# Optimization experiments

Measured on AMD Instinct MI355X. Metric: run time of the kernel, lower is better.

Reference implementation:

```python
import jax, jax.numpy as jnp
import numpy as np

BN_EPS = 1e-5


def _get_normals(radius, nsample, xyz):
    # xyz: [B, N, 3] -> normals [B, N, 3] (eigenvector of smallest eigenvalue)
    B, N, _ = xyz.shape
    sq = jnp.sum(xyz * xyz, axis=-1)                      # [B, N]
    sqrdists = sq[:, :, None] + sq[:, None, :] - 2.0 * jnp.einsum('bnc,bmc->bnm', xyz, xyz)
    ar = jnp.arange(N, dtype=jnp.int32)
    group_idx = jnp.where(sqrdists > radius * radius, N, ar[None, None, :])  # [B, N, N]
    group_idx = jnp.sort(group_idx, axis=-1)[:, :, :nsample]                 # [B, N, ns]
    group_idx = jnp.where(group_idx == N, group_idx[:, :, :1], group_idx)
    group_points = jax.vmap(lambda pts, idx: pts[idx])(xyz, group_idx)       # [B, N, ns, 3]
    centered = group_points - group_points.mean(axis=2, keepdims=True)
    cov = jnp.einsum('bnsc,bnsd->bncd', centered, centered)                  # [B, N, 3, 3]
    _, eigen_vectors = jnp.linalg.eigh(cov)
    return eigen_vectors[..., 0]


def _conv_bn(h, w, b, g, be, m, v, relu=True):
    # h: [B, N, Cin]; 1x1 Conv1d == per-point linear; BN in eval mode
    h = h @ w.T + b
    h = (h - m) / jnp.sqrt(v + BN_EPS) * g + be
    return jax.nn.relu(h) if relu else h


def setup_inputs() -> dict:
    key = jax.random.key(0)
    ks = jax.random.split(key, 32)
    B, N = 4, 4096
    inp = {
        'x': jax.random.uniform(ks[0], (B, N, 3), dtype=jnp.float32),
        'small': 0.2,
        'large': 0.3,
    }
    chans = [(1, 16), (16, 32), (32, 16), (16, 1)]
    for li, (cin, cout) in enumerate(chans, start=1):
        k = 4 * li
        inp[f'w{li}'] = jax.random.normal(ks[k], (cout, cin), dtype=jnp.float32) * (1.0 / np.sqrt(cin))
        inp[f'b{li}'] = jax.random.normal(ks[k + 1], (cout,), dtype=jnp.float32) * 0.1
        inp[f'g{li}'] = jax.random.uniform(ks[k + 2], (cout,), dtype=jnp.float32) + 0.5
        inp[f'be{li}'] = jax.random.normal(ks[k + 3], (cout,), dtype=jnp.float32) * 0.1
        inp[f'm{li}'] = jnp.zeros((cout,), dtype=jnp.float32)
        inp[f'v{li}'] = jnp.ones((cout,), dtype=jnp.float32)
    return inp


def reference(x, small, large,
              w1, b1, g1, be1, m1, v1,
              w2, b2, g2, be2, m2, v2,
              w3, b3, g3, be3, m3, v3,
              w4, b4, g4, be4, m4, v4):
    xyz = x[:, :, :3]
    small_n = _get_normals(small, 32, xyz)   # [B, N, 3]
    large_n = _get_normals(large, 64, xyz)
    curvature = jnp.linalg.norm((small_n - large_n) * 0.5, axis=2)  # [B, N]
    h = curvature[..., None]                                        # [B, N, 1]
    h = _conv_bn(h, w1, b1, g1, be1, m1, v1)
    h = _conv_bn(h, w2, b2, g2, be2, m2, v2)
    h = _conv_bn(h, w3, b3, g3, be3, m3, v3)
    h = _conv_bn(h, w4, b4, g4, be4, m4, v4, relu=False)
    return h[..., 0]                                                # [B, N]
```

## Files before the change

### kernel.cpp

```cpp
#include <hip/hip_runtime.h>
#include <math.h>

#define BLAS_FMA 1
#define SYR2_VARIANT 0

#define DEV static __device__ __forceinline__

DEV float fA(float a, float b){ return __fadd_rn(a,b); }
DEV float fSb(float a, float b){ return __fsub_rn(a,b); }
DEV float fM(float a, float b){ return __fmul_rn(a,b); }
DEV float fDv(float a, float b){ return __fdiv_rn(a,b); }
DEV float fQ(float a){ return __fsqrt_rn(a); }
DEV float fF(float a, float b, float c){ return __builtin_fmaf(a,b,c); }
DEV float fSGN(float a, float b){ return copysignf(a,b); }

DEV float slapy2f(float x, float y){
  float xa=fabsf(x), ya=fabsf(y);
  float w=fmaxf(xa,ya), z=fminf(xa,ya);
  if (z==0.0f) return w;
  float t=fDv(z,w);
  return fM(w, fQ(fA(1.0f, fM(t,t))));
}

DEV void slartgf(float f, float g, float* c, float* s, float* r){
  const float safmin=1.17549435e-38f;
  const float safmax=8.50705917e+37f;
  const float rtmin=1.08420217e-19f;
  const float rtmax=6.52169543e+18f;
  float f1=fabsf(f), g1=fabsf(g);
  if (g==0.0f){ *c=1.0f; *s=0.0f; *r=f; }
  else if (f==0.0f){ *c=0.0f; *s=fSGN(1.0f,g); *r=g1; }
  else {
    if (f1>rtmin && f1<rtmax && g1>rtmin && g1<rtmax){
      float d=fQ(fA(fM(f,f), fM(g,g)));
      *c=fDv(f1,d);
      *r=fSGN(d,f);
      *s=fDv(g,*r);
    } else {
      float u=fminf(safmax, fmaxf(safmin, fmaxf(f1,g1)));
      float fs=fDv(f,u), gs=fDv(g,u);
      float d=fQ(fA(fM(fs,fs), fM(gs,gs)));
      *c=fDv(fabsf(fs), d);
      *r=fSGN(d,f);
      *s=fDv(gs,*r);
      *r=fM(*r,u);
    }
  }
}

DEV void slaev2f(float a, float b, float c, float* rt1, float* rt2, float* cs1, float* sn1){
  float sm=fA(a,c);
  float df=fSb(a,c);
  float adf=fabsf(df);
  float tb=fA(b,b);
  float ab=fabsf(tb);
  float acmx, acmn;
  if (fabsf(a)>fabsf(c)){ acmx=a; acmn=c; } else { acmx=c; acmn=a; }
  float rt;
  if (adf>ab){ float t=fDv(ab,adf); rt=fM(adf, fQ(fA(1.0f, fM(t,t)))); }
  else if (adf<ab){ float t=fDv(adf,ab); rt=fM(ab, fQ(fA(1.0f, fM(t,t)))); }
  else { rt=fM(ab, fQ(2.0f)); }
  int sgn1;
  if (sm<0.0f){
    *rt1=fM(0.5f, fSb(sm,rt)); sgn1=-1;
    *rt2=fSb(fM(fDv(acmx,*rt1),acmn), fM(fDv(b,*rt1),b));
  } else if (sm>0.0f){
    *rt1=fM(0.5f, fA(sm,rt)); sgn1=1;
    *rt2=fSb(fM(fDv(acmx,*rt1),acmn), fM(fDv(b,*rt1),b));
  } else {
    *rt1=fM(0.5f,rt); *rt2=fM(-0.5f,rt); sgn1=1;
  }
  float cs; int sgn2;
  if (df>=0.0f){ cs=fA(df,rt); sgn2=1; } else { cs=fSb(df,rt); sgn2=-1; }
  float acs=fabsf(cs);
  if (acs>ab){
    float ct=fDv(-tb,cs);
    *sn1=fDv(1.0f, fQ(fA(1.0f, fM(ct,ct))));
    *cs1=fM(ct,*sn1);
  } else {
    if (ab==0.0f){ *cs1=1.0f; *sn1=0.0f; }
    else {
      float tn=fDv(-cs,tb);
      *cs1=fDv(1.0f, fQ(fA(1.0f, fM(tn,tn))));
      *sn1=fM(tn,*cs1);
    }
  }
  if (sgn1==sgn2){ float tn=*cs1; *cs1=-(*sn1); *sn1=tn; }
}

DEV void eig3_smallest(float a00, float a10, float a20, float a11, float a21, float a22,
                       float* vout){
  const float RMIN=3.13916472e-16f;
  const float RMAX=3.18559313e+15f;
  float anrm=fmaxf(fabsf(a00), fmaxf(fabsf(a10), fmaxf(fabsf(a20),
             fmaxf(fabsf(a11), fmaxf(fabsf(a21), fabsf(a22))))));
  if (anrm>0.0f && anrm<RMIN){
    float sig=fDv(RMIN,anrm);
    a00=fM(a00,sig); a10=fM(a10,sig); a20=fM(a20,sig);
    a11=fM(a11,sig); a21=fM(a21,sig); a22=fM(a22,sig);
  } else if (anrm>RMAX){
    float sig=fDv(RMAX,anrm);
    a00=fM(a00,sig); a10=fM(a10,sig); a20=fM(a20,sig);
    a11=fM(a11,sig); a21=fM(a21,sig); a22=fM(a22,sig);
  }
  float d[3], e[2];
  float tau1=0.0f, hv2=0.0f;
  {
    float xnorm=fabsf(a20);
    if (xnorm==0.0f){
      tau1=0.0f;
      d[0]=a00; d[1]=a11; d[2]=a22;
      e[0]=a10; e[1]=a21;
    } else {
      float alpha=a10;
      float beta=-fSGN(slapy2f(alpha,xnorm), alpha);
      tau1=fDv(fSb(beta,alpha), beta);
      float rs=fDv(1.0f, fSb(alpha,beta));
      hv2=fM(a20, rs);
      float t2a=fM(a21, hv2);
#if BLAS_FMA
      float w1=fF(tau1, t2a, fM(tau1, a11));
      float w2=fF(fM(tau1,hv2), a22, fM(tau1, a21));
      float sd=fF(hv2, w2, w1);
#else
      float w1=fA(fM(tau1,a11), fM(tau1,t2a));
      float w2=fA(fM(tau1,a21), fM(fM(tau1,hv2),a22));
      float sd=fA(w1, fM(w2,hv2));
#endif
      float al2=fM(fM(-0.5f,tau1), sd);
      float nw1=fA(w1, al2);
#if BLAS_FMA
      float nw2=fF(al2, hv2, w2);
#else
      float nw2=fA(w2, fM(al2,hv2));
#endif
      w1=nw1; w2=nw2;
      float b11, b21, b22;
#if SYR2_VARIANT==0
      b11=fA(a11, fM(-2.0f, w1));
      b21=fA(a21, fF(hv2, -w1, -w2));
      b22=fA(a22, fF(hv2, -w2, fM(w2, -hv2)));
#elif SYR2_VARIANT==1
      b11=fSb(fSb(a11, w1), w1);
      b21=fSb(fF(hv2, -w1, a21), w2);
      b22=fF(w2, -hv2, fF(hv2, -w2, a22));
#else
      b11=fA(fA(a11, -w1), -w1);
      b21=fA(fA(a21, fM(hv2,-w1)), -w2);
      b22=fA(fA(a22, fM(hv2,-w2)), fM(w2,-hv2));
#endif
      d[0]=a00; d[1]=b11; d[2]=b22;
      e[0]=beta; e[1]=b21;
    }
  }
  float z[9]={1.0f,0.0f,0.0f, 0.0f,1.0f,0.0f, 0.0f,0.0f,1.0f};
  const float EPS=5.96046448e-08f;
  const float EPS2=3.55271368e-15f;
  const float SAFMIN=1.17549435e-38f;
  const float SSFMAX=3.07445735e+18f;
  const float SSFMIN=3.05175781e-05f;
  int l1=1, jtot=0; const int nmaxit=90;
  bool skip_sort=false;
  while (l1<=3){
    if (l1>1) e[l1-2]=0.0f;
    int m=3;
    for (int mm=l1; mm<=2; ++mm){
      float tst=fabsf(e[mm-1]);
      if (tst==0.0f){ m=mm; break; }
      if (tst<=fM(fM(fQ(fabsf(d[mm-1])), fQ(fabsf(d[mm]))), EPS)){ e[mm-1]=0.0f; m=mm; break; }
    }
    int l=l1, lsv=l, lend=m, lendsv=m;
    l1=m+1;
    if (lend==l) continue;
    float anorm=fabsf(d[lend-1]);
    for (int i=l; i<=lend-1; ++i){ anorm=fmaxf(anorm,fabsf(d[i-1])); anorm=fmaxf(anorm,fabsf(e[i-1])); }
    if (anorm==0.0f) continue;
    int iscale=0;
    if (anorm>SSFMAX){
      iscale=1; float mv=fDv(SSFMAX,anorm);
      for (int i=l;i<=lend;++i) d[i-1]=fM(d[i-1],mv);
      for (int i=l;i<=lend-1;++i) e[i-1]=fM(e[i-1],mv);
    } else if (anorm<SSFMIN){
      iscale=2; float mv=fDv(SSFMIN,anorm);
      for (int i=l;i<=lend;++i) d[i-1]=fM(d[i-1],mv);
      for (int i=l;i<=lend-1;++i) e[i-1]=fM(e[i-1],mv);
    }
    if (fabsf(d[lend-1])<fabsf(d[l-1])){ lend=lsv; l=lendsv; }
    if (lend>l){
      for (;;){
        int M=lend;
        if (l!=lend){
          for (int mm=l; mm<=lend-1; ++mm){
            float ee=fabsf(e[mm-1]);
            float tst=fM(ee,ee);
            if (tst<=fA(fM(fM(EPS2,fabsf(d[mm-1])), fabsf(d[mm])), SAFMIN)){ M=mm; break; }
          }
        }
        if (M<lend) e[M-1]=0.0f;
        float p=d[l-1];
        if (M==l){
          l+=1;
          if (l<=lend) continue; else break;
        }
        if (M==l+1){
          float rt1,rt2,cc,ss;
          slaev2f(d[l-1], e[l-1], d[l], &rt1,&rt2,&cc,&ss);
          for (int i=0;i<3;++i){
            float t=z[i+3*l];
            z[i+3*l]    =fSb(fM(cc,t), fM(ss,z[i+3*(l-1)]));
            z[i+3*(l-1)]=fA (fM(ss,t), fM(cc,z[i+3*(l-1)]));
          }
          d[l-1]=rt1; d[l]=rt2; e[l-1]=0.0f; l+=2;
          if (l<=lend) continue; else break;
        }
        if (jtot==nmaxit) break;
        ++jtot;
        float g=fDv(fSb(d[l],p), fM(2.0f,e[l-1]));
        float r=slapy2f(g,1.0f);
        g=fA(fSb(d[M-1],p), fDv(e[l-1], fA(g, fSGN(r,g))));
        float s=1.0f, c=1.0f; p=0.0f;
        float cst[2], sst[2];
        for (int i=M-1; i>=l; --i){
          float f=fM(s,e[i-1]);
          float bb=fM(c,e[i-1]);
          slartgf(g,f,&c,&s,&r);
          if (i!=M-1) e[i]=r;
          g=fSb(d[i],p);
          r=fA(fM(fSb(d[i-1],g),s), fM(fM(2.0f,c),bb));
          p=fM(s,r);
          d[i]=fA(g,p);
          g=fSb(fM(c,r),bb);
          cst[i-l]=c; sst[i-l]=-s;
        }
        int nr=M-l;
        for (int j=nr; j>=1; --j){
          float ct=cst[j-1], st=sst[j-1];
          if (ct!=1.0f || st!=0.0f){
            int c0=(l-1)+(j-1);
            for (int i=0;i<3;++i){
              float t=z[i+3*(c0+1)];
              z[i+3*(c0+1)]=fSb(fM(ct,t), fM(st,z[i+3*c0]));
              z[i+3*c0]    =fA (fM(st,t), fM(ct,z[i+3*c0]));
            }
          }
        }
        d[l-1]=fSb(d[l-1],p);
        e[l-1]=g;
      }
    } else {
      for (;;){
        int M=lend;
        if (l!=lend){
          for (int mm=l; mm>=lend+1; --mm){
            float ee=fabsf(e[mm-2]);
            float tst=fM(ee,ee);
            if (tst<=fA(fM(fM(EPS2,fabsf(d[mm-1])), fabsf(d[mm-2])), SAFMIN)){ M=mm; break; }
          }
        }
        if (M>lend) e[M-2]=0.0f;
        float p=d[l-1];
        if (M==l){
          l-=1;
          if (l>=lend) continue; else break;
        }
        if (M==l-1){
          float rt1,rt2,cc,ss;
          slaev2f(d[l-2], e[l-2], d[l-1], &rt1,&rt2,&cc,&ss);
          for (int i=0;i<3;++i){
            float t=z[i+3*(l-1)];
            z[i+3*(l-1)]=fSb(fM(cc,t), fM(ss,z[i+3*(l-2)]));
            z[i+3*(l-2)]=fA (fM(ss,t), fM(cc,z[i+3*(l-2)]));
          }
          d[l-2]=rt1; d[l-1]=rt2; e[l-2]=0.0f; l-=2;
          if (l>=lend) continue; else break;
        }
        if (jtot==nmaxit) break;
        ++jtot;
        float g=fDv(fSb(d[l-2],p), fM(2.0f,e[l-2]));
        float r=slapy2f(g,1.0f);
        g=fA(fSb(d[M-1],p), fDv(e[l-2], fA(g, fSGN(r,g))));
        float s=1.0f, c=1.0f; p=0.0f;
        float cst[2], sst[2];
        for (int i=M; i<=l-1; ++i){
          float f=fM(s,e[i-1]);
          float bb=fM(c,e[i-1]);
          slartgf(g,f,&c,&s,&r);
          if (i!=M) e[i-2]=r;
          g=fSb(d[i-1],p);
          r=fA(fM(fSb(d[i],g),s), fM(fM(2.0f,c),bb));
          p=fM(s,r);
          d[i-1]=fA(g,p);
          g=fSb(fM(c,r),bb);
          cst[i-M]=c; sst[i-M]=s;
        }
        int nr=l-M;
        for (int j=1; j<=nr; ++j){
          float ct=cst[j-1], st=sst[j-1];
          if (ct!=1.0f || st!=0.0f){
            int c0=(M-1)+(j-1);
            for (int i=0;i<3;++i){
              float t=z[i+3*(c0+1)];
              z[i+3*(c0+1)]=fSb(fM(ct,t), fM(st,z[i+3*c0]));
              z[i+3*c0]    =fA(fM(st,t), fM(ct,z[i+3*c0]));
            }
          }
        }
        d[l-1]=fSb(d[l-1],p);
        e[l-2]=g;
      }
    }
    if (iscale==1){
      float mv=fDv(anorm,SSFMAX);
      for (int i=lsv;i<=lendsv;++i) d[i-1]=fM(d[i-1],mv);
      for (int i=lsv;i<=lendsv-1;++i) e[i-1]=fM(e[i-1],mv);
    } else if (iscale==2){
      float mv=fDv(anorm,SSFMIN);
      for (int i=lsv;i<=lendsv;++i) d[i-1]=fM(d[i-1],mv);
      for (int i=lsv;i<=lendsv-1;++i) e[i-1]=fM(e[i-1],mv);
    }
    if (jtot>=nmaxit){ skip_sort=true; break; }
  }
  if (!skip_sort){
    for (int ii=2; ii<=3; ++ii){
      int i=ii-1, k=i; float p=d[i-1];
      for (int j=ii; j<=3; ++j) if (d[j-1]<p){ k=j; p=d[j-1]; }
      if (k!=i){
        d[k-1]=d[i-1]; d[i-1]=p;
        for (int row=0; row<3; ++row){
          float t=z[row+3*(i-1)]; z[row+3*(i-1)]=z[row+3*(k-1)]; z[row+3*(k-1)]=t;
        }
      }
    }
  }
  float z0=z[0], z1=z[1], z2=z[2];
  if (tau1!=0.0f){
#if BLAS_FMA
    float wv=fF(hv2, z2, z1);
    float t2=fM(-tau1, wv);
    z1=fA(z1, t2);
    z2=fF(t2, hv2, z2);
#else
    float wv=fA(z1, fM(z2,hv2));
    float t2=fM(-tau1, wv);
    z1=fA(z1, t2);
    z2=fA(z2, fM(hv2,t2));
#endif
  }
  vout[0]=z0; vout[1]=z1; vout[2]=z2;
}

struct KP {
  const float* x; const float* rs; const float* rl;
  const float *w1,*b1,*g1,*be1,*m1,*v1;
  const float *w2,*b2,*g2,*be2,*m2,*v2;
  const float *w3,*b3,*g3,*be3,*m3,*v3;
  const float *w4,*b4,*g4,*be4,*m4,*v4;
  float* out;
};

#define WS_STRIDE 128

__global__ __launch_bounds__(64) void scan_kernel(const float* __restrict__ x,
                                                  const float* __restrict__ rsp,
                                                  const float* __restrict__ rlp,
                                                  unsigned short* __restrict__ ws){
  const int lane=threadIdx.x;
  const int pt=blockIdx.x;
  const int b=pt>>12, n=pt&4095;
  const float* P=x+(size_t)b*(4096*3);
  const double rds=rint((double)rsp[0]*1e7)/1e7;
  const double rdl=rint((double)rlp[0]*1e7)/1e7;
  const float rr_s=(float)(rds*rds);
  const float rr_l=(float)(rdl*rdl);
  const float px=P[3*n], py=P[3*n+1], pz=P[3*n+2];
  const float sqn=fA(fA(fM(px,px),fM(py,py)),fM(pz,pz));
  unsigned short* w=ws+(size_t)pt*WS_STRIDE;
  int cs=0, cl=0;
  for (int c=0;c<64;++c){
    int j=c*64+lane;
    float qx=P[3*j], qy=P[3*j+1], qz=P[3*j+2];
    float sqj=fA(fA(fM(qx,qx),fM(qy,qy)),fM(qz,qz));
    float dot=fA(fA(fM(px,qx),fM(py,qy)),fM(pz,qz));
    float d2=fSb(fA(sqn,sqj), fM(2.0f,dot));
    bool pl=!(d2>rr_l);
    bool ps=!(d2>rr_s);
    unsigned long long bl=__ballot(pl);
    unsigned long long bs=__ballot(ps);
    unsigned long long ltm=(1ull<<lane)-1ull;
    int posl=cl+__popcll(bl&ltm);
    int poss=cs+__popcll(bs&ltm);
    if (pl&&posl<64) w[posl]=(unsigned short)j;
    if (ps&&poss<32) w[64+poss]=(unsigned short)j;
    cl+=__popcll(bl); if(cl>64) cl=64;
    cs+=__popcll(bs); if(cs>32) cs=32;
    if (cs>=32&&cl>=64) break;
  }
  if (lane==0){ w[96]=(unsigned short)cl; w[97]=(unsigned short)cs; }
}

__global__ __launch_bounds__(64) void moments_kernel(const float* __restrict__ x,
                                                     const unsigned short* __restrict__ ws,
                                                     float* __restrict__ covB){
  __shared__ float sP[4096*3];
  __shared__ unsigned int sWu[64*65];
  const int lane=threadIdx.x;
  const int base=blockIdx.x*64;
  const int b=base>>12;
  const float* P=x+(size_t)b*(4096*3);
  {
    const float4* src=(const float4*)P;
    float4* dst=(float4*)sP;
    for (int i=lane;i<4096*3/4;i+=64) dst[i]=src[i];
  }
  {
    const unsigned int* wsrc=(const unsigned int*)(ws+(size_t)base*WS_STRIDE);
    for (int i=lane;i<64*64;i+=64){
      int row=i>>6, col=i&63;
      sWu[row*65+col]=wsrc[i];
    }
  }
  __syncthreads();

  const unsigned short* sW16=(const unsigned short*)sWu;
  const int rbase=lane*130;
  const int cln=sW16[rbase+96], csn=sW16[rbase+97];
  const int j0l=sW16[rbase+0],  j0s=sW16[rbase+64];

  float ssx=0.0f,ssy=0.0f,ssz=0.0f, slx=0.0f,sly=0.0f,slz=0.0f;
#pragma unroll 16
  for (int k=0;k<32;++k){
    int idx=(k<csn)?(int)sW16[rbase+64+k]:j0s;
    ssx=fA(ssx,sP[3*idx]); ssy=fA(ssy,sP[3*idx+1]); ssz=fA(ssz,sP[3*idx+2]);
  }
#pragma unroll 16
  for (int k=0;k<64;++k){
    int idx=(k<cln)?(int)sW16[rbase+k]:j0l;
    slx=fA(slx,sP[3*idx]); sly=fA(sly,sP[3*idx+1]); slz=fA(slz,sP[3*idx+2]);
  }
  const float msx=fDv(ssx,32.0f), msy=fDv(ssy,32.0f), msz=fDv(ssz,32.0f);
  const float mlx=fDv(slx,64.0f), mly=fDv(sly,64.0f), mlz=fDv(slz,64.0f);

  float sc0=0,sc1=0,sc2=0,sc3=0,sc4=0,sc5=0;
#pragma unroll 16
  for (int k=0;k<32;++k){
    int idx=(k<csn)?(int)sW16[rbase+64+k]:j0s;
    float cx=fSb(sP[3*idx],msx), cy=fSb(sP[3*idx+1],msy), cz=fSb(sP[3*idx+2],msz);
    sc0=fA(sc0,fM(cx,cx)); sc1=fA(sc1,fM(cy,cx)); sc2=fA(sc2,fM(cz,cx));
    sc3=fA(sc3,fM(cy,cy)); sc4=fA(sc4,fM(cz,cy)); sc5=fA(sc5,fM(cz,cz));
  }
  float lc0=0,lc1=0,lc2=0,lc3=0,lc4=0,lc5=0;
#pragma unroll 16
  for (int k=0;k<64;++k){
    int idx=(k<cln)?(int)sW16[rbase+k]:j0l;
    float cx=fSb(sP[3*idx],mlx), cy=fSb(sP[3*idx+1],mly), cz=fSb(sP[3*idx+2],mlz);
    lc0=fA(lc0,fM(cx,cx)); lc1=fA(lc1,fM(cy,cx)); lc2=fA(lc2,fM(cz,cx));
    lc3=fA(lc3,fM(cy,cy)); lc4=fA(lc4,fM(cz,cy)); lc5=fA(lc5,fM(cz,cz));
  }

  float* cb=covB+(size_t)(base+lane)*12;
  cb[0]=sc0; cb[1]=sc1; cb[2]=sc2; cb[3]=sc3; cb[4]=sc4; cb[5]=sc5;
  cb[6]=lc0; cb[7]=lc1; cb[8]=lc2; cb[9]=lc3; cb[10]=lc4; cb[11]=lc5;
}

__global__ __launch_bounds__(64) void eigmlp_kernel(KP kp, const float* __restrict__ covB){
  __shared__ float sN[32][3];
  const int lane=threadIdx.x;
  const int g=lane>>1;
  const int t=blockIdx.x*32+g;
  const int p=t>>1, which=t&1;
  const float* cb=covB+(size_t)p*12+which*6;
  float v[3];
  eig3_smallest(cb[0],cb[1],cb[2],cb[3],cb[4],cb[5],v);
  if ((lane&1)==0){ sN[g][0]=v[0]; sN[g][1]=v[1]; sN[g][2]=v[2]; }
  __syncthreads();

  if (lane<16){
    const int pt=blockIdx.x*16+lane;
    const float* sn=sN[2*lane];
    const float* ln=sN[2*lane+1];
    float dx=fM(fSb(sn[0],ln[0]),0.5f);
    float dy=fM(fSb(sn[1],ln[1]),0.5f);
    float dz=fM(fSb(sn[2],ln[2]),0.5f);
    float curv=fQ(fA(fA(fM(dx,dx),fM(dy,dy)),fM(dz,dz)));

    float h1[16];
#pragma unroll
    for (int j=0;j<16;++j){
      float a0=fA(fM(kp.w1[j],curv), kp.b1[j]);
      a0=fA(fM(fDv(fSb(a0,kp.m1[j]), fQ(fA(kp.v1[j],1e-5f))), kp.g1[j]), kp.be1[j]);
      h1[j]=fmaxf(a0,0.0f);
    }
    float h2[32];
#pragma unroll
    for (int j=0;j<32;++j){
      float a0=0.0f;
#pragma unroll
      for (int k=0;k<16;++k) a0=fF(h1[k], kp.w2[j*16+k], a0);
      a0=fA(a0, kp.b2[j]);
      a0=fA(fM(fDv(fSb(a0,kp.m2[j]), fQ(fA(kp.v2[j],1e-5f))), kp.g2[j]), kp.be2[j]);
      h2[j]=fmaxf(a0,0.0f);
    }
    float h3[16];
#pragma unroll
    for (int j=0;j<16;++j){
      float a0=0.0f;
#pragma unroll
      for (int k=0;k<32;++k) a0=fF(h2[k], kp.w3[j*32+k], a0);
      a0=fA(a0, kp.b3[j]);
      a0=fA(fM(fDv(fSb(a0,kp.m3[j]), fQ(fA(kp.v3[j],1e-5f))), kp.g3[j]), kp.be3[j]);
      h3[j]=fmaxf(a0,0.0f);
    }
    float o=0.0f;
#pragma unroll
    for (int k=0;k<16;++k) o=fF(h3[k], kp.w4[k], o);
    o=fA(o, kp.b4[0]);
    o=fA(fM(fDv(fSb(o,kp.m4[0]), fQ(fA(kp.v4[0],1e-5f))), kp.g4[0]), kp.be4[0]);
    kp.out[pt]=o;
  }
}

__global__ __launch_bounds__(256) void freq_kernel(KP kp){
  __shared__ float sP[4096*3];
  __shared__ float sSq[4096];
  __shared__ unsigned short sIdxL[64][66];
  __shared__ unsigned short sIdxS[64][34];
  __shared__ unsigned char sCntL[64], sCntS[64];
  const int tid=threadIdx.x;
  const int lane=tid&63, wid=tid>>6;
  const int b=blockIdx.x>>6;
  const int n0=(blockIdx.x&63)*64;
  const float* P=kp.x+(size_t)b*(4096*3);
  for (int i=tid;i<4096*3;i+=256) sP[i]=P[i];
  for (int j=tid;j<4096;j+=256){
    float qx=P[3*j],qy=P[3*j+1],qz=P[3*j+2];
    sSq[j]=fA(fA(fM(qx,qx),fM(qy,qy)),fM(qz,qz));
  }
  __syncthreads();
  const double rds=rint((double)kp.rs[0]*1e7)/1e7;
  const double rdl=rint((double)kp.rl[0]*1e7)/1e7;
  const float rr_s=(float)(rds*rds);
  const float rr_l=(float)(rdl*rdl);
  for (int pi=0; pi<16; ++pi){
    const int pl_i=wid*16+pi;
    const int n=n0+pl_i;
    const float px=sP[3*n], py=sP[3*n+1], pz=sP[3*n+2];
    const float sqn=sSq[n];
    int cs=0, cl=0;
    for (int c=0;c<64;++c){
      int j=c*64+lane;
      float dot=fA(fA(fM(px,sP[3*j]),fM(py,sP[3*j+1])),fM(pz,sP[3*j+2]));
      float d2=fSb(fA(sqn,sSq[j]), fM(2.0f,dot));
      bool pl_=!(d2>rr_l);
      bool ps_=!(d2>rr_s);
      unsigned long long bl=__ballot(pl_);
      unsigned long long bs=__ballot(ps_);
      unsigned long long ltm=(1ull<<lane)-1ull;
      int posl=cl+__popcll(bl&ltm);
      int poss=cs+__popcll(bs&ltm);
      if (pl_&&posl<64) sIdxL[pl_i][posl]=(unsigned short)j;
      if (ps_&&poss<32) sIdxS[pl_i][poss]=(unsigned short)j;
      cl+=__popcll(bl); if(cl>64) cl=64;
      cs+=__popcll(bs); if(cs>32) cs=32;
      if (cs>=32&&cl>=64) break;
    }
    if (lane==0){ sCntL[pl_i]=(unsigned char)cl; sCntS[pl_i]=(unsigned char)cs; }
  }
  __syncthreads();
  if (lane<16){
    const int pl_i=wid*16+lane;
    const int ptg=blockIdx.x*64+pl_i;
    const int csn=sCntS[pl_i], cln=sCntL[pl_i];
    const int j0s=sIdxS[pl_i][0], j0l=sIdxL[pl_i][0];
    float ssx=0.0f,ssy=0.0f,ssz=0.0f, slx=0.0f,sly=0.0f,slz=0.0f;
    for (int k=0;k<32;++k){
      int idx=(k<csn)?(int)sIdxS[pl_i][k]:j0s;
      ssx=fA(ssx,sP[3*idx]); ssy=fA(ssy,sP[3*idx+1]); ssz=fA(ssz,sP[3*idx+2]);
    }
    for (int k=0;k<64;++k){
      int idx=(k<cln)?(int)sIdxL[pl_i][k]:j0l;
      slx=fA(slx,sP[3*idx]); sly=fA(sly,sP[3*idx+1]); slz=fA(slz,sP[3*idx+2]);
    }
    const float msx=fDv(ssx,32.0f), msy=fDv(ssy,32.0f), msz=fDv(ssz,32.0f);
    const float mlx=fDv(slx,64.0f), mly=fDv(sly,64.0f), mlz=fDv(slz,64.0f);
    float sc0=0,sc1=0,sc2=0,sc3=0,sc4=0,sc5=0;
    for (int k=0;k<32;++k){
      int idx=(k<csn)?(int)sIdxS[pl_i][k]:j0s;
      float cx=fSb(sP[3*idx],msx), cy=fSb(sP[3*idx+1],msy), cz=fSb(sP[3*idx+2],msz);
      sc0=fA(sc0,fM(cx,cx)); sc1=fA(sc1,fM(cy,cx)); sc2=fA(sc2,fM(cz,cx));
      sc3=fA(sc3,fM(cy,cy)); sc4=fA(sc4,fM(cz,cy)); sc5=fA(sc5,fM(cz,cz));
    }
    float lc0=0,lc1=0,lc2=0,lc3=0,lc4=0,lc5=0;
    for (int k=0;k<64;++k){
      int idx=(k<cln)?(int)sIdxL[pl_i][k]:j0l;
      float cx=fSb(sP[3*idx],mlx), cy=fSb(sP[3*idx+1],mly), cz=fSb(sP[3*idx+2],mlz);
      lc0=fA(lc0,fM(cx,cx)); lc1=fA(lc1,fM(cy,cx)); lc2=fA(lc2,fM(cz,cx));
      lc3=fA(lc3,fM(cy,cy)); lc4=fA(lc4,fM(cz,cy)); lc5=fA(lc5,fM(cz,cz));
    }
    float snv[3], lnv[3];
    eig3_smallest(sc0,sc1,sc2,sc3,sc4,sc5, snv);
    eig3_smallest(lc0,lc1,lc2,lc3,lc4,lc5, lnv);
    float dx=fM(fSb(snv[0],lnv[0]),0.5f);
    float dy=fM(fSb(snv[1],lnv[1]),0.5f);
    float dz=fM(fSb(snv[2],lnv[2]),0.5f);
    float curv=fQ(fA(fA(fM(dx,dx),fM(dy,dy)),fM(dz,dz)));
    float h1[16];
#pragma unroll
    for (int j=0;j<16;++j){
      float a0=fA(fM(kp.w1[j],curv), kp.b1[j]);
      a0=fA(fM(fDv(fSb(a0,kp.m1[j]), fQ(fA(kp.v1[j],1e-5f))), kp.g1[j]), kp.be1[j]);
      h1[j]=fmaxf(a0,0.0f);
    }
    float h2[32];
#pragma unroll
    for (int j=0;j<32;++j){
      float a0=0.0f;
#pragma unroll
      for (int k=0;k<16;++k) a0=fF(h1[k], kp.w2[j*16+k], a0);
      a0=fA(a0, kp.b2[j]);
      a0=fA(fM(fDv(fSb(a0,kp.m2[j]), fQ(fA(kp.v2[j],1e-5f))), kp.g2[j]), kp.be2[j]);
      h2[j]=fmaxf(a0,0.0f);
    }
    float h3[16];
#pragma unroll
    for (int j=0;j<16;++j){
      float a0=0.0f;
#pragma unroll
      for (int k=0;k<32;++k) a0=fF(h2[k], kp.w3[j*32+k], a0);
      a0=fA(a0, kp.b3[j]);
      a0=fA(fM(fDv(fSb(a0,kp.m3[j]), fQ(fA(kp.v3[j],1e-5f))), kp.g3[j]), kp.be3[j]);
      h3[j]=fmaxf(a0,0.0f);
    }
    float o=0.0f;
#pragma unroll
    for (int k=0;k<16;++k) o=fF(h3[k], kp.w4[k], o);
    o=fA(o, kp.b4[0]);
    o=fA(fM(fDv(fSb(o,kp.m4[0]), fQ(fA(kp.v4[0],1e-5f))), kp.g4[0]), kp.be4[0]);
    kp.out[ptg]=o;
  }
}

extern "C" void kernel_launch(void* const* d_in, const int* in_sizes, int n_in,
                              void* d_out, int out_size, void* d_ws, size_t ws_size,
                              hipStream_t stream){
  (void)n_in; (void)out_size;
  KP kp;
  kp.x  =(const float*)d_in[0];
  kp.rs =(const float*)d_in[1];
  kp.rl =(const float*)d_in[2];
  kp.w1 =(const float*)d_in[3];  kp.b1 =(const float*)d_in[4];  kp.g1 =(const float*)d_in[5];
  kp.be1=(const float*)d_in[6];  kp.m1 =(const float*)d_in[7];  kp.v1 =(const float*)d_in[8];
  kp.w2 =(const float*)d_in[9];  kp.b2 =(const float*)d_in[10]; kp.g2 =(const float*)d_in[11];
  kp.be2=(const float*)d_in[12]; kp.m2 =(const float*)d_in[13]; kp.v2 =(const float*)d_in[14];
  kp.w3 =(const float*)d_in[15]; kp.b3 =(const float*)d_in[16]; kp.g3 =(const float*)d_in[17];
  kp.be3=(const float*)d_in[18]; kp.m3 =(const float*)d_in[19]; kp.v3 =(const float*)d_in[20];
  kp.w4 =(const float*)d_in[21]; kp.b4 =(const float*)d_in[22]; kp.g4 =(const float*)d_in[23];
  kp.be4=(const float*)d_in[24]; kp.m4 =(const float*)d_in[25]; kp.v4 =(const float*)d_in[26];
  kp.out=(float*)d_out;
  const int BN=in_sizes[0]/3;
  const size_t ws_need=(size_t)BN*(256+48);
  if (ws_size>=ws_need){
    unsigned short* wsA=(unsigned short*)d_ws;
    float* covB=(float*)((char*)d_ws + (size_t)BN*256);
    scan_kernel<<<BN, 64, 0, stream>>>(kp.x, kp.rs, kp.rl, wsA);
    moments_kernel<<<BN/64, 64, 0, stream>>>(kp.x, wsA, covB);
    eigmlp_kernel<<<BN/16, 64, 0, stream>>>(kp, covB);
  } else {
    freq_kernel<<<BN/64, 256, 0, stream>>>(kp);
  }
}
```

Baseline: 195.0 us.

## Drop multi-kernel workspace path and always launch fused freq kernel

Removes the scan/moments/eig-MLP three-kernel pipeline that staged neighbor indices and covariances through global workspace, and always launches the single fused kernel. This avoids workspace round trips and extra launches. In exchange it has fewer blocks (one per 64 points) and more work per block, which may underuse the GPU.

```diff
diff --git a/kernel.cpp b/kernel.cpp
--- a/kernel.cpp
+++ b/kernel.cpp
@@ -358,167 +358,6 @@
   float* out;
 };
 
-#define WS_STRIDE 128
-
-__global__ __launch_bounds__(64) void scan_kernel(const float* __restrict__ x,
-                                                  const float* __restrict__ rsp,
-                                                  const float* __restrict__ rlp,
-                                                  unsigned short* __restrict__ ws){
-  const int lane=threadIdx.x;
-  const int pt=blockIdx.x;
-  const int b=pt>>12, n=pt&4095;
-  const float* P=x+(size_t)b*(4096*3);
-  const double rds=rint((double)rsp[0]*1e7)/1e7;
-  const double rdl=rint((double)rlp[0]*1e7)/1e7;
-  const float rr_s=(float)(rds*rds);
-  const float rr_l=(float)(rdl*rdl);
-  const float px=P[3*n], py=P[3*n+1], pz=P[3*n+2];
-  const float sqn=fA(fA(fM(px,px),fM(py,py)),fM(pz,pz));
-  unsigned short* w=ws+(size_t)pt*WS_STRIDE;
-  int cs=0, cl=0;
-  for (int c=0;c<64;++c){
-    int j=c*64+lane;
-    float qx=P[3*j], qy=P[3*j+1], qz=P[3*j+2];
-    float sqj=fA(fA(fM(qx,qx),fM(qy,qy)),fM(qz,qz));
-    float dot=fA(fA(fM(px,qx),fM(py,qy)),fM(pz,qz));
-    float d2=fSb(fA(sqn,sqj), fM(2.0f,dot));
-    bool pl=!(d2>rr_l);
-    bool ps=!(d2>rr_s);
-    unsigned long long bl=__ballot(pl);
-    unsigned long long bs=__ballot(ps);
-    unsigned long long ltm=(1ull<<lane)-1ull;
-    int posl=cl+__popcll(bl&ltm);
-    int poss=cs+__popcll(bs&ltm);
-    if (pl&&posl<64) w[posl]=(unsigned short)j;
-    if (ps&&poss<32) w[64+poss]=(unsigned short)j;
-    cl+=__popcll(bl); if(cl>64) cl=64;
-    cs+=__popcll(bs); if(cs>32) cs=32;
-    if (cs>=32&&cl>=64) break;
-  }
-  if (lane==0){ w[96]=(unsigned short)cl; w[97]=(unsigned short)cs; }
-}
-
-__global__ __launch_bounds__(64) void moments_kernel(const float* __restrict__ x,
-                                                     const unsigned short* __restrict__ ws,
-                                                     float* __restrict__ covB){
-  __shared__ float sP[4096*3];
-  __shared__ unsigned int sWu[64*65];
-  const int lane=threadIdx.x;
-  const int base=blockIdx.x*64;
-  const int b=base>>12;
-  const float* P=x+(size_t)b*(4096*3);
-  {
-    const float4* src=(const float4*)P;
-    float4* dst=(float4*)sP;
-    for (int i=lane;i<4096*3/4;i+=64) dst[i]=src[i];
-  }
-  {
-    const unsigned int* wsrc=(const unsigned int*)(ws+(size_t)base*WS_STRIDE);
-    for (int i=lane;i<64*64;i+=64){
-      int row=i>>6, col=i&63;
-      sWu[row*65+col]=wsrc[i];
-    }
-  }
-  __syncthreads();
-
-  const unsigned short* sW16=(const unsigned short*)sWu;
-  const int rbase=lane*130;
-  const int cln=sW16[rbase+96], csn=sW16[rbase+97];
-  const int j0l=sW16[rbase+0],  j0s=sW16[rbase+64];
-
-  float ssx=0.0f,ssy=0.0f,ssz=0.0f, slx=0.0f,sly=0.0f,slz=0.0f;
-#pragma unroll 16
-  for (int k=0;k<32;++k){
-    int idx=(k<csn)?(int)sW16[rbase+64+k]:j0s;
-    ssx=fA(ssx,sP[3*idx]); ssy=fA(ssy,sP[3*idx+1]); ssz=fA(ssz,sP[3*idx+2]);
-  }
-#pragma unroll 16
-  for (int k=0;k<64;++k){
-    int idx=(k<cln)?(int)sW16[rbase+k]:j0l;
-    slx=fA(slx,sP[3*idx]); sly=fA(sly,sP[3*idx+1]); slz=fA(slz,sP[3*idx+2]);
-  }
-  const float msx=fDv(ssx,32.0f), msy=fDv(ssy,32.0f), msz=fDv(ssz,32.0f);
-  const float mlx=fDv(slx,64.0f), mly=fDv(sly,64.0f), mlz=fDv(slz,64.0f);
-
-  float sc0=0,sc1=0,sc2=0,sc3=0,sc4=0,sc5=0;
-#pragma unroll 16
-  for (int k=0;k<32;++k){
-    int idx=(k<csn)?(int)sW16[rbase+64+k]:j0s;
-    float cx=fSb(sP[3*idx],msx), cy=fSb(sP[3*idx+1],msy), cz=fSb(sP[3*idx+2],msz);
-    sc0=fA(sc0,fM(cx,cx)); sc1=fA(sc1,fM(cy,cx)); sc2=fA(sc2,fM(cz,cx));
-    sc3=fA(sc3,fM(cy,cy)); sc4=fA(sc4,fM(cz,cy)); sc5=fA(sc5,fM(cz,cz));
-  }
-  float lc0=0,lc1=0,lc2=0,lc3=0,lc4=0,lc5=0;
-#pragma unroll 16
-  for (int k=0;k<64;++k){
-    int idx=(k<cln)?(int)sW16[rbase+k]:j0l;
-    float cx=fSb(sP[3*idx],mlx), cy=fSb(sP[3*idx+1],mly), cz=fSb(sP[3*idx+2],mlz);
-    lc0=fA(lc0,fM(cx,cx)); lc1=fA(lc1,fM(cy,cx)); lc2=fA(lc2,fM(cz,cx));
-    lc3=fA(lc3,fM(cy,cy)); lc4=fA(lc4,fM(cz,cy)); lc5=fA(lc5,fM(cz,cz));
-  }
-
-  float* cb=covB+(size_t)(base+lane)*12;
-  cb[0]=sc0; cb[1]=sc1; cb[2]=sc2; cb[3]=sc3; cb[4]=sc4; cb[5]=sc5;
-  cb[6]=lc0; cb[7]=lc1; cb[8]=lc2; cb[9]=lc3; cb[10]=lc4; cb[11]=lc5;
-}
-
-__global__ __launch_bounds__(64) void eigmlp_kernel(KP kp, const float* __restrict__ covB){
-  __shared__ float sN[32][3];
-  const int lane=threadIdx.x;
-  const int g=lane>>1;
-  const int t=blockIdx.x*32+g;
-  const int p=t>>1, which=t&1;
-  const float* cb=covB+(size_t)p*12+which*6;
-  float v[3];
-  eig3_smallest(cb[0],cb[1],cb[2],cb[3],cb[4],cb[5],v);
-  if ((lane&1)==0){ sN[g][0]=v[0]; sN[g][1]=v[1]; sN[g][2]=v[2]; }
-  __syncthreads();
-
-  if (lane<16){
-    const int pt=blockIdx.x*16+lane;
-    const float* sn=sN[2*lane];
-    const float* ln=sN[2*lane+1];
-    float dx=fM(fSb(sn[0],ln[0]),0.5f);
-    float dy=fM(fSb(sn[1],ln[1]),0.5f);
-    float dz=fM(fSb(sn[2],ln[2]),0.5f);
-    float curv=fQ(fA(fA(fM(dx,dx),fM(dy,dy)),fM(dz,dz)));
-
-    float h1[16];
-#pragma unroll
-    for (int j=0;j<16;++j){
-      float a0=fA(fM(kp.w1[j],curv), kp.b1[j]);
-      a0=fA(fM(fDv(fSb(a0,kp.m1[j]), fQ(fA(kp.v1[j],1e-5f))), kp.g1[j]), kp.be1[j]);
-      h1[j]=fmaxf(a0,0.0f);
-    }
-    float h2[32];
-#pragma unroll
-    for (int j=0;j<32;++j){
-      float a0=0.0f;
-#pragma unroll
-      for (int k=0;k<16;++k) a0=fF(h1[k], kp.w2[j*16+k], a0);
-      a0=fA(a0, kp.b2[j]);
-      a0=fA(fM(fDv(fSb(a0,kp.m2[j]), fQ(fA(kp.v2[j],1e-5f))), kp.g2[j]), kp.be2[j]);
-      h2[j]=fmaxf(a0,0.0f);
-    }
-    float h3[16];
-#pragma unroll
-    for (int j=0;j<16;++j){
-      float a0=0.0f;
-#pragma unroll
-      for (int k=0;k<32;++k) a0=fF(h2[k], kp.w3[j*32+k], a0);
-      a0=fA(a0, kp.b3[j]);
-      a0=fA(fM(fDv(fSb(a0,kp.m3[j]), fQ(fA(kp.v3[j],1e-5f))), kp.g3[j]), kp.be3[j]);
-      h3[j]=fmaxf(a0,0.0f);
-    }
-    float o=0.0f;
-#pragma unroll
-    for (int k=0;k<16;++k) o=fF(h3[k], kp.w4[k], o);
-    o=fA(o, kp.b4[0]);
-    o=fA(fM(fDv(fSb(o,kp.m4[0]), fQ(fA(kp.v4[0],1e-5f))), kp.g4[0]), kp.be4[0]);
-    kp.out[pt]=o;
-  }
-}
-
 __global__ __launch_bounds__(256) void freq_kernel(KP kp){
   __shared__ float sP[4096*3];
   __shared__ float sSq[4096];
@@ -642,7 +481,7 @@
 extern "C" void kernel_launch(void* const* d_in, const int* in_sizes, int n_in,
                               void* d_out, int out_size, void* d_ws, size_t ws_size,
                               hipStream_t stream){
-  (void)n_in; (void)out_size;
+  (void)n_in; (void)out_size; (void)d_ws; (void)ws_size;
   KP kp;
   kp.x  =(const float*)d_in[0];
   kp.rs =(const float*)d_in[1];
@@ -657,14 +496,5 @@
   kp.be4=(const float*)d_in[24]; kp.m4 =(const float*)d_in[25]; kp.v4 =(const float*)d_in[26];
   kp.out=(float*)d_out;
   const int BN=in_sizes[0]/3;
-  const size_t ws_need=(size_t)BN*(256+48);
-  if (ws_size>=ws_need){
-    unsigned short* wsA=(unsigned short*)d_ws;
-    float* covB=(float*)((char*)d_ws + (size_t)BN*256);
-    scan_kernel<<<BN, 64, 0, stream>>>(kp.x, kp.rs, kp.rl, wsA);
-    moments_kernel<<<BN/64, 64, 0, stream>>>(kp.x, wsA, covB);
-    eigmlp_kernel<<<BN/16, 64, 0, stream>>>(kp, covB);
-  } else {
-    freq_kernel<<<BN/64, 256, 0, stream>>>(kp);
-  }
+  freq_kernel<<<BN/64, 256, 0, stream>>>(kp);
 }
```

Measured after the change: 258.2 us. 1.32x slower.

## Split moments per point into two threads and drop LDS point staging

Applied to the files above, without the earlier changes.

The moments kernel now assigns one thread per (point, radius) pair instead of one thread per point handling both radii, which doubles the grid. It also stops copying the whole 4096-point cloud and the neighbour-index records into shared memory, and instead loads each thread's index record with vector loads and gathers coordinates straight from global memory through the cache. The aim is to remove the large per-block LDS fill (48KB per block), which limits occupancy, and to shorten the serial work per thread. The cost is uncoalesced global gathers and a warp-uniform 64-trip loop in which small-radius threads mask off half the iterations.

```diff
diff --git a/kernel.cpp b/kernel.cpp
--- a/kernel.cpp
+++ b/kernel.cpp
@@ -398,68 +398,55 @@
   if (lane==0){ w[96]=(unsigned short)cl; w[97]=(unsigned short)cs; }
 }
 
-__global__ __launch_bounds__(64) void moments_kernel(const float* __restrict__ x,
-                                                     const unsigned short* __restrict__ ws,
-                                                     float* __restrict__ covB){
-  __shared__ float sP[4096*3];
-  __shared__ unsigned int sWu[64*65];
+__global__ __launch_bounds__(64) void moments2_kernel(const float* __restrict__ x,
+                                                      const unsigned short* __restrict__ ws,
+                                                      float* __restrict__ covB){
   const int lane=threadIdx.x;
-  const int base=blockIdx.x*64;
-  const int b=base>>12;
+  const int t=blockIdx.x*64+lane;
+  const int p=t>>1, which=t&1;
+  const int b=p>>12;
   const float* P=x+(size_t)b*(4096*3);
-  {
-    const float4* src=(const float4*)P;
-    float4* dst=(float4*)sP;
-    for (int i=lane;i<4096*3/4;i+=64) dst[i]=src[i];
-  }
-  {
-    const unsigned int* wsrc=(const unsigned int*)(ws+(size_t)base*WS_STRIDE);
-    for (int i=lane;i<64*64;i+=64){
-      int row=i>>6, col=i&63;
-      sWu[row*65+col]=wsrc[i];
-    }
-  }
-  __syncthreads();
-
-  const unsigned short* sW16=(const unsigned short*)sWu;
-  const int rbase=lane*130;
-  const int cln=sW16[rbase+96], csn=sW16[rbase+97];
-  const int j0l=sW16[rbase+0],  j0s=sW16[rbase+64];
-
-  float ssx=0.0f,ssy=0.0f,ssz=0.0f, slx=0.0f,sly=0.0f,slz=0.0f;
-#pragma unroll 16
-  for (int k=0;k<32;++k){
-    int idx=(k<csn)?(int)sW16[rbase+64+k]:j0s;
-    ssx=fA(ssx,sP[3*idx]); ssy=fA(ssy,sP[3*idx+1]); ssz=fA(ssz,sP[3*idx+2]);
-  }
-#pragma unroll 16
+  const unsigned char* recB=(const unsigned char*)(ws+(size_t)p*WS_STRIDE);
+  const uint4* q=(const uint4*)(recB + (which? 0 : 128));
+  uint4 v0=q[0], v1=q[1], v2=q[2], v3=q[3];
+  uint4 v4=q[4], v5=q[5], v6=q[6], v7=q[7];
+  const unsigned int cw=*(const unsigned int*)(recB+192);
+  const int cnt = which? (int)(cw&0xFFFFu) : (int)(cw>>16);
+  const int trip= which? 64 : 32;
+  unsigned int a[32]={v0.x,v0.y,v0.z,v0.w, v1.x,v1.y,v1.z,v1.w,
+                      v2.x,v2.y,v2.z,v2.w, v3.x,v3.y,v3.z,v3.w,
+                      v4.x,v4.y,v4.z,v4.w, v5.x,v5.y,v5.z,v5.w,
+                      v6.x,v6.y,v6.z,v6.w, v7.x,v7.y,v7.z,v7.w};
+  const int j0=(int)(a[0]&0xFFFFu);
+
+  float sx=0.0f, sy=0.0f, sz=0.0f;
+#pragma unroll
   for (int k=0;k<64;++k){
-    int idx=(k<cln)?(int)sW16[rbase+k]:j0l;
-    slx=fA(slx,sP[3*idx]); sly=fA(sly,sP[3*idx+1]); slz=fA(slz,sP[3*idx+2]);
-  }
-  const float msx=fDv(ssx,32.0f), msy=fDv(ssy,32.0f), msz=fDv(ssz,32.0f);
-  const float mlx=fDv(slx,64.0f), mly=fDv(sly,64.0f), mlz=fDv(slz,64.0f);
-
-  float sc0=0,sc1=0,sc2=0,sc3=0,sc4=0,sc5=0;
-#pragma unroll 16
-  for (int k=0;k<32;++k){
-    int idx=(k<csn)?(int)sW16[rbase+64+k]:j0s;
-    float cx=fSb(sP[3*idx],msx), cy=fSb(sP[3*idx+1],msy), cz=fSb(sP[3*idx+2],msz);
-    sc0=fA(sc0,fM(cx,cx)); sc1=fA(sc1,fM(cy,cx)); sc2=fA(sc2,fM(cz,cx));
-    sc3=fA(sc3,fM(cy,cy)); sc4=fA(sc4,fM(cz,cy)); sc5=fA(sc5,fM(cz,cz));
-  }
-  float lc0=0,lc1=0,lc2=0,lc3=0,lc4=0,lc5=0;
-#pragma unroll 16
+    int raw=(k&1)? (int)(a[k>>1]>>16) : (int)(a[k>>1]&0xFFFFu);
+    int idx=(k<cnt)? raw : j0;
+    float cx=P[3*idx], cy=P[3*idx+1], cz=P[3*idx+2];
+    float nx=fA(sx,cx), ny=fA(sy,cy), nz=fA(sz,cz);
+    bool en=(k<trip);
+    sx=en?nx:sx; sy=en?ny:sy; sz=en?nz:sz;
+  }
+  const float dv=which? 64.0f : 32.0f;
+  const float mx=fDv(sx,dv), my=fDv(sy,dv), mz=fDv(sz,dv);
+
+  float c0=0,c1=0,c2=0,c3=0,c4=0,c5=0;
+#pragma unroll
   for (int k=0;k<64;++k){
-    int idx=(k<cln)?(int)sW16[rbase+k]:j0l;
-    float cx=fSb(sP[3*idx],mlx), cy=fSb(sP[3*idx+1],mly), cz=fSb(sP[3*idx+2],mlz);
-    lc0=fA(lc0,fM(cx,cx)); lc1=fA(lc1,fM(cy,cx)); lc2=fA(lc2,fM(cz,cx));
-    lc3=fA(lc3,fM(cy,cy)); lc4=fA(lc4,fM(cz,cy)); lc5=fA(lc5,fM(cz,cz));
-  }
-
-  float* cb=covB+(size_t)(base+lane)*12;
-  cb[0]=sc0; cb[1]=sc1; cb[2]=sc2; cb[3]=sc3; cb[4]=sc4; cb[5]=sc5;
-  cb[6]=lc0; cb[7]=lc1; cb[8]=lc2; cb[9]=lc3; cb[10]=lc4; cb[11]=lc5;
+    int raw=(k&1)? (int)(a[k>>1]>>16) : (int)(a[k>>1]&0xFFFFu);
+    int idx=(k<cnt)? raw : j0;
+    float cx=fSb(P[3*idx],mx), cy=fSb(P[3*idx+1],my), cz=fSb(P[3*idx+2],mz);
+    float t0=fA(c0,fM(cx,cx)), t1=fA(c1,fM(cy,cx)), t2=fA(c2,fM(cz,cx));
+    float t3=fA(c3,fM(cy,cy)), t4=fA(c4,fM(cz,cy)), t5=fA(c5,fM(cz,cz));
+    bool en=(k<trip);
+    c0=en?t0:c0; c1=en?t1:c1; c2=en?t2:c2;
+    c3=en?t3:c3; c4=en?t4:c4; c5=en?t5:c5;
+  }
+
+  float* cb=covB+(size_t)p*12+which*6;
+  cb[0]=c0; cb[1]=c1; cb[2]=c2; cb[3]=c3; cb[4]=c4; cb[5]=c5;
 }
 
 __global__ __launch_bounds__(64) void eigmlp_kernel(KP kp, const float* __restrict__ covB){
@@ -662,7 +649,7 @@
     unsigned short* wsA=(unsigned short*)d_ws;
     float* covB=(float*)((char*)d_ws + (size_t)BN*256);
     scan_kernel<<<BN, 64, 0, stream>>>(kp.x, kp.rs, kp.rl, wsA);
-    moments_kernel<<<BN/64, 64, 0, stream>>>(kp.x, wsA, covB);
+    moments2_kernel<<<BN/32, 64, 0, stream>>>(kp.x, wsA, covB);
     eigmlp_kernel<<<BN/16, 64, 0, stream>>>(kp, covB);
   } else {
     freq_kernel<<<BN/64, 256, 0, stream>>>(kp);
```

Measured after the change: 182.3 us. -6.5%, faster.
